# Kernel tuning notes

Hardware: AMD Instinct MI355X
Metric: run time of the kernel (lower is better)

The kernel has to match this reference:

```python
import jax, jax.numpy as jnp
import numpy as np

B, T, C, H = 4, 1024, 1024, 16
D = C // H  # head dim = 64


def setup_inputs() -> dict:
    key = jax.random.key(0)
    ks = jax.random.split(key, 12)
    s = 1.0 / np.sqrt(C)
    inp = {
        "x": jax.random.normal(ks[0], (B, T, C), jnp.float32),
        "Wq": jax.random.normal(ks[1], (C, C), jnp.float32) * s,
        "bq": jnp.zeros((C,), jnp.float32),
        "Wk": jax.random.normal(ks[2], (C, C), jnp.float32) * s,
        "bk": jnp.zeros((C,), jnp.float32),
        "Wv": jax.random.normal(ks[3], (C, C), jnp.float32) * s,
        "bv": jnp.zeros((C,), jnp.float32),
        "time_weighting": jnp.ones((H, T, T), jnp.float32),
        "head_mix_w": jax.random.normal(ks[4], (H, H), jnp.float32) * (1.0 / np.sqrt(H)),
        "Wp": jax.random.normal(ks[5], (C, C), jnp.float32) * s,
        "bp": jnp.zeros((C,), jnp.float32),
    }
    return inp


def reference(x, Wq, bq, Wk, bk, Wv, bv, time_weighting, head_mix_w, Wp, bp):
    Bx, Tx, Cx = x.shape
    half = Cx // 2
    # time_shift: first half of channels sees x shifted by one step (row 0 -> zeros)
    x_shift = jnp.pad(x, ((0, 0), (1, 0), (0, 0)))[:, :Tx, :half]
    xs = jnp.concatenate([x_shift, x[:, :, half:]], axis=-1)

    def heads(y):  # [B,T,C] -> [B,H,T,D]
        return y.reshape(Bx, Tx, H, D).transpose(0, 2, 1, 3)

    q = heads(xs @ Wq.T + bq)
    k = heads(xs @ Wk.T + bk)
    v = heads(xs @ Wv.T + bv)

    att = jnp.einsum("bhtd,bhsd->bhts", q, k) * (1.0 / np.sqrt(D))
    causal = jnp.tril(jnp.ones((Tx, Tx), bool))
    att = jnp.where(causal, att, -jnp.inf)
    att = jax.nn.softmax(att, axis=-1)
    att = att * time_weighting[:, :Tx, :Tx]
    # 1x1 conv across heads
    att = jnp.einsum("oh,bhts->bots", head_mix_w, att)

    y = jnp.einsum("bhts,bhsd->bhtd", att, v)
    y = y.transpose(0, 2, 1, 3).reshape(Bx, Tx, Cx)
    return y @ Wp.T + bp
```

## Files before the change

### kernel.cpp

```cpp
#include <hip/hip_runtime.h>
#include <hip/hip_bf16.h>

#define T_ 1024

typedef __attribute__((ext_vector_type(8))) short short8;
typedef __attribute__((ext_vector_type(4))) float f32x4;
typedef __bf16 bf16x8 __attribute__((ext_vector_type(8)));
typedef __attribute__((ext_vector_type(4))) unsigned short ushort4v;

__device__ __forceinline__ unsigned short f2bf(float f) {
    unsigned u = __float_as_uint(f);
    u += 0x7fffu + ((u >> 16) & 1u);
    return (unsigned short)(u >> 16);
}
__device__ __forceinline__ float bf2f(unsigned short s) {
    return __uint_as_float(((unsigned)s) << 16);
}
__device__ __forceinline__ unsigned short f2h(float f) {
    _Float16 h = (_Float16)f;
    return __builtin_bit_cast(unsigned short, h);
}
__device__ __forceinline__ float h2f(unsigned short u) {
    return (float)__builtin_bit_cast(_Float16, u);
}

__device__ __forceinline__ void gload16(const unsigned short* g, unsigned short* l) {
    __builtin_amdgcn_global_load_lds((const __attribute__((address_space(1))) unsigned int*)g,
                                     (__attribute__((address_space(3))) unsigned int*)l,
                                     16, 0, 0);
}

__global__ __launch_bounds__(256) void k_convert(
    const float* __restrict__ s0, const float* __restrict__ s1,
    const float* __restrict__ s2, const float* __restrict__ s3,
    unsigned short* __restrict__ d0, unsigned short* __restrict__ d1,
    unsigned short* __restrict__ d2, unsigned short* __restrict__ d3) {
    const float* src; unsigned short* dst;
    switch (blockIdx.y) {
        case 0:  src = s0; dst = d0; break;
        case 1:  src = s1; dst = d1; break;
        case 2:  src = s2; dst = d2; break;
        default: src = s3; dst = d3; break;
    }
    int i = (blockIdx.x * 256 + threadIdx.x) * 4;
    float4 v = *(const float4*)(src + i);
    ushort4v ov = { f2bf(v.x), f2bf(v.y), f2bf(v.z), f2bf(v.w) };
    *(ushort4v*)(dst + i) = ov;
}

__global__ __launch_bounds__(256) void k_xs(const float* __restrict__ x,
                                            unsigned short* __restrict__ xs) {
    int idx = (blockIdx.x * 256 + threadIdx.x) * 4;
    int c = idx & 1023;
    int m = idx >> 10;
    int t = m & 1023;
    float4 v;
    if (c < 512) {
        if (t == 0) { v.x = v.y = v.z = v.w = 0.f; }
        else        { v = *(const float4*)(x + (size_t)(m - 1) * 1024 + c); }
    } else {
        v = *(const float4*)(x + (size_t)m * 1024 + c);
    }
    ushort4v ov = { f2bf(v.x), f2bf(v.y), f2bf(v.z), f2bf(v.w) };
    *(ushort4v*)(xs + (size_t)m * 1024 + c) = ov;
}

__device__ __forceinline__ void gemm_body(const unsigned short* __restrict__ A,
                                          const unsigned short* __restrict__ Bt,
                                          int m0, int n0, int tid, f32x4 acc[4][4],
                                          unsigned short (*As)[32], unsigned short (*Bs)[32]) {
    const int lane = tid & 63, w = tid >> 6;
    const int wr = w >> 1, wc = w & 1;
    const int srow = lane >> 2;
    const int scp  = lane & 3;
#pragma unroll
    for (int i = 0; i < 4; i++)
#pragma unroll
        for (int j = 0; j < 4; j++) acc[i][j] = (f32x4){0.f, 0.f, 0.f, 0.f};

    for (int k0 = 0; k0 < 1024; k0 += 32) {
        __syncthreads();
#pragma unroll
        for (int it = 0; it < 2; it++) {
            int base = it * 64 + w * 16;
            int row = base + srow;
            int c2 = scp ^ ((row >> 1) & 3);
            gload16(A + (size_t)(m0 + row) * 1024 + k0 + c2 * 8, &As[base][0]);
            gload16(Bt + (size_t)(n0 + row) * 1024 + k0 + c2 * 8, &Bs[base][0]);
        }
        __syncthreads();
        bf16x8 af[4], bg[4];
        int c = lane >> 4;
#pragma unroll
        for (int i = 0; i < 4; i++) {
            int row = wr * 64 + i * 16 + (lane & 15);
            af[i] = *(const bf16x8*)&As[row][(c ^ ((row >> 1) & 3)) * 8];
        }
#pragma unroll
        for (int j = 0; j < 4; j++) {
            int row = wc * 64 + j * 16 + (lane & 15);
            bg[j] = *(const bf16x8*)&Bs[row][(c ^ ((row >> 1) & 3)) * 8];
        }
#pragma unroll
        for (int i = 0; i < 4; i++)
#pragma unroll
            for (int j = 0; j < 4; j++)
                acc[i][j] = __builtin_amdgcn_mfma_f32_16x16x32_bf16(af[i], bg[j], acc[i][j], 0, 0, 0);
    }
}

__global__ __launch_bounds__(256) void k_gemm_qkv(
    const unsigned short* __restrict__ A,
    const unsigned short* __restrict__ wq, const unsigned short* __restrict__ wk,
    const unsigned short* __restrict__ wv,
    const float* __restrict__ bq, const float* __restrict__ bk, const float* __restrict__ bv,
    unsigned short* __restrict__ qo, unsigned short* __restrict__ ko,
    unsigned short* __restrict__ vo) {
    __shared__ unsigned short As[128][32];
    __shared__ unsigned short Bs[128][32];
    const int mat = blockIdx.y >> 3;
    const unsigned short* Bt = mat == 0 ? wq : (mat == 1 ? wk : wv);
    const float* bias = mat == 0 ? bq : (mat == 1 ? bk : bv);
    unsigned short* out = mat == 0 ? qo : (mat == 1 ? ko : vo);
    const int m0 = blockIdx.x * 128, n0 = (blockIdx.y & 7) * 128;
    const int tid = threadIdx.x, lane = tid & 63, w = tid >> 6;
    const int wr = w >> 1, wc = w & 1;
    f32x4 acc[4][4];
    gemm_body(A, Bt, m0, n0, tid, acc, As, Bs);
#pragma unroll
    for (int i = 0; i < 4; i++) {
        int mbase = m0 + wr * 64 + i * 16 + ((lane >> 4) << 2);
#pragma unroll
        for (int j = 0; j < 4; j++) {
            int n = n0 + wc * 64 + j * 16 + (lane & 15);
            float bv_ = bias[n];
            int h = n >> 6, d = n & 63;
#pragma unroll
            for (int r = 0; r < 4; r++) {
                int mm = mbase + r;
                int b = mm >> 10, t = mm & 1023;
                out[(size_t)((b * 16 + h) * 1024 + t) * 64 + d] = f2bf(acc[i][j][r] + bv_);
            }
        }
    }
}

__global__ __launch_bounds__(256) void k_gemm_out(
    const unsigned short* __restrict__ A, const unsigned short* __restrict__ Bt,
    const float* __restrict__ bias, float* __restrict__ out) {
    __shared__ unsigned short As[128][32];
    __shared__ unsigned short Bs[128][32];
    const int m0 = blockIdx.x * 128, n0 = blockIdx.y * 128;
    const int tid = threadIdx.x, lane = tid & 63, w = tid >> 6;
    const int wr = w >> 1, wc = w & 1;
    f32x4 acc[4][4];
    gemm_body(A, Bt, m0, n0, tid, acc, As, Bs);
#pragma unroll
    for (int i = 0; i < 4; i++) {
        int mbase = m0 + wr * 64 + i * 16 + ((lane >> 4) << 2);
#pragma unroll
        for (int j = 0; j < 4; j++) {
            int n = n0 + wc * 64 + j * 16 + (lane & 15);
            float bv_ = bias[n];
#pragma unroll
            for (int r = 0; r < 4; r++)
                out[(size_t)(mbase + r) * 1024 + n] = acc[i][j][r] + bv_;
        }
    }
}

__global__ __launch_bounds__(256) void k_scores(const unsigned short* __restrict__ qb,
                                                const unsigned short* __restrict__ kb,
                                                unsigned short* __restrict__ Eb,
                                                float* __restrict__ invb) {
    __shared__ unsigned short qs[64][64];
    __shared__ unsigned short ks[64][64];
    const int tid = threadIdx.x, lane = tid & 63, w = tid >> 6;
    const int t0 = (15 - (int)blockIdx.x) * 64;
    const int bh = blockIdx.y;
    const unsigned short* qp = qb + (size_t)bh * 65536;
    const unsigned short* kp = kb + (size_t)bh * 65536;

#pragma unroll
    for (int it = 0; it < 2; it++) {
        int ch = it * 256 + tid; int row = ch >> 3, c = ch & 7;
        *(short8*)&qs[row][(c ^ (row & 7)) * 8] = *(const short8*)(qp + (size_t)(t0 + row) * 64 + c * 8);
    }
    __syncthreads();
    const int row_a = w * 16 + (lane & 15);
    bf16x8 a0 = *(const bf16x8*)&qs[row_a][(((lane >> 4)    ) ^ (row_a & 7)) * 8];
    bf16x8 a1 = *(const bf16x8*)&qs[row_a][(((lane >> 4) + 4) ^ (row_a & 7)) * 8];
    const int tr = t0 + w * 16 + ((lane >> 4) << 2);
    float l_[4] = {0.f, 0.f, 0.f, 0.f};
    unsigned short* ep = Eb + (size_t)bh * ((size_t)T_ * T_);

    for (int s0 = 0; s0 <= t0 + 63; s0 += 64) {
        __syncthreads();
#pragma unroll
        for (int it = 0; it < 2; it++) {
            int ch = it * 256 + tid; int row = ch >> 3, c = ch & 7;
            *(short8*)&ks[row][(c ^ (row & 7)) * 8] = *(const short8*)(kp + (size_t)(s0 + row) * 64 + c * 8);
        }
        __syncthreads();
        f32x4 S[4];
#pragma unroll
        for (int sf = 0; sf < 4; sf++) {
            int row = sf * 16 + (lane & 15);
            bf16x8 b0 = *(const bf16x8*)&ks[row][(((lane >> 4)    ) ^ (row & 7)) * 8];
            bf16x8 b1 = *(const bf16x8*)&ks[row][(((lane >> 4) + 4) ^ (row & 7)) * 8];
            f32x4 z = (f32x4){0.f, 0.f, 0.f, 0.f};
            z = __builtin_amdgcn_mfma_f32_16x16x32_bf16(a0, b0, z, 0, 0, 0);
            z = __builtin_amdgcn_mfma_f32_16x16x32_bf16(a1, b1, z, 0, 0, 0);
            S[sf] = z;
        }
#pragma unroll
        for (int sf = 0; sf < 4; sf++) {
            int s = s0 + sf * 16 + (lane & 15);
#pragma unroll
            for (int r = 0; r < 4; r++) {
                float es = (s <= tr + r) ? __expf(S[sf][r] * 0.125f) : 0.f;
                l_[r] += es;
                ep[(size_t)(tr + r) * T_ + s] = f2h(es);
            }
        }
    }
#pragma unroll
    for (int r = 0; r < 4; r++) {
        float ts = l_[r];
        ts += __shfl_xor(ts, 1);
        ts += __shfl_xor(ts, 2);
        ts += __shfl_xor(ts, 4);
        ts += __shfl_xor(ts, 8);
        l_[r] = ts;
    }
    if ((lane & 15) == 0) {
#pragma unroll
        for (int r = 0; r < 4; r++) invb[(size_t)bh * T_ + tr + r] = 1.f / l_[r];
    }
}

__global__ __launch_bounds__(256) void k_mix6(unsigned short* __restrict__ Sb,
                                              const float* __restrict__ invb,
                                              const float* __restrict__ tw,
                                              const float* __restrict__ mixw) {
    const int t = blockIdx.x, b = blockIdx.y;
    const int send = t | 63;
    const int tid = threadIdx.x;
    __shared__ float mw[256];
    __shared__ float inv_s[16];
    mw[tid] = mixw[tid];
    if (tid < 16) inv_s[tid] = invb[(size_t)(b * 16 + tid) * T_ + t];
    __syncthreads();

    const int s4 = tid * 4;
    if (s4 > send) return;
    unsigned short* plane0 = Sb + (size_t)b * 16 * 1048576;
    const unsigned rowb = (unsigned)t * 1024u + (unsigned)s4;

    ushort4v e[16];
    float4 tv[16];
#pragma unroll
    for (int h = 0; h < 16; h++)
        e[h] = *(const ushort4v*)(plane0 + (size_t)h * 1048576 + rowb);
#pragma unroll
    for (int h = 0; h < 16; h++)
        tv[h] = *(const float4*)(tw + (size_t)h * 1048576 + rowb);

    float p[16][4];
#pragma unroll
    for (int h = 0; h < 16; h++) {
        float iv = inv_s[h];
        p[h][0] = h2f(e[h].x) * iv * tv[h].x;
        p[h][1] = h2f(e[h].y) * iv * tv[h].y;
        p[h][2] = h2f(e[h].z) * iv * tv[h].z;
        p[h][3] = h2f(e[h].w) * iv * tv[h].w;
    }

#pragma unroll
    for (int o = 0; o < 16; o++) {
        float a0 = 0.f, a1 = 0.f, a2 = 0.f, a3 = 0.f;
#pragma unroll
        for (int h = 0; h < 16; h++) {
            float m = mw[o * 16 + h];
            a0 += m * p[h][0];
            a1 += m * p[h][1];
            a2 += m * p[h][2];
            a3 += m * p[h][3];
        }
        ushort4v pk = { f2bf(a0), f2bf(a1), f2bf(a2), f2bf(a3) };
        *(ushort4v*)(plane0 + (size_t)o * 1048576 + rowb) = pk;
    }
}

__global__ __launch_bounds__(256) void k_av(const unsigned short* __restrict__ att,
                                            const unsigned short* __restrict__ vb,
                                            unsigned short* __restrict__ y1) {
    __shared__ unsigned short as_[64][64];
    __shared__ unsigned short vs[64][72];
    const int tid = threadIdx.x, lane = tid & 63, w = tid >> 6;
    const int t0 = (15 - (int)blockIdx.x) * 64;
    const int bh = blockIdx.y;
    const int b = bh >> 4, h = bh & 15;
    const unsigned short* ap = att + (size_t)bh * 1048576;
    const unsigned short* vp = vb + (size_t)bh * 65536;
    f32x4 acc[4];
#pragma unroll
    for (int j = 0; j < 4; j++) acc[j] = (f32x4){0.f, 0.f, 0.f, 0.f};

    for (int s0 = 0; s0 <= t0 + 63; s0 += 64) {
        __syncthreads();
#pragma unroll
        for (int it = 0; it < 2; it++) {
            int ch = it * 256 + tid;
            int row = ch >> 3, c = ch & 7;
            *(short8*)&as_[row][(c ^ (row & 7)) * 8] =
                *(const short8*)(ap + (size_t)(t0 + row) * 1024 + s0 + c * 8);
            int sp = ch >> 3, dc = (ch & 7) * 8;
            short8 vv = *(const short8*)(vp + (size_t)(s0 + sp) * 64 + dc);
#pragma unroll
            for (int i = 0; i < 8; i++) vs[dc + i][sp] = ((unsigned short*)&vv)[i];
        }
        __syncthreads();
        const int row_a = w * 16 + (lane & 15);
#pragma unroll
        for (int ks = 0; ks < 2; ks++) {
            bf16x8 af = *(const bf16x8*)&as_[row_a][((((lane >> 4) + 4 * ks)) ^ (row_a & 7)) * 8];
#pragma unroll
            for (int j = 0; j < 4; j++) {
                bf16x8 bg = *(const bf16x8*)&vs[j * 16 + (lane & 15)][ks * 32 + (lane >> 4) * 8];
                acc[j] = __builtin_amdgcn_mfma_f32_16x16x32_bf16(af, bg, acc[j], 0, 0, 0);
            }
        }
    }

    int t = t0 + w * 16 + ((lane >> 4) << 2);
#pragma unroll
    for (int j = 0; j < 4; j++) {
        int d = j * 16 + (lane & 15);
#pragma unroll
        for (int r = 0; r < 4; r++)
            y1[(size_t)(b * 1024 + t + r) * 1024 + h * 64 + d] = f2bf(acc[j][r]);
    }
}

extern "C" void kernel_launch(void* const* d_in, const int* in_sizes, int n_in,
                              void* d_out, int out_size, void* d_ws, size_t ws_size,
                              hipStream_t stream) {
    (void)in_sizes; (void)n_in; (void)out_size; (void)ws_size;
    const float* x    = (const float*)d_in[0];
    const float* Wq   = (const float*)d_in[1];
    const float* bq   = (const float*)d_in[2];
    const float* Wk   = (const float*)d_in[3];
    const float* bk   = (const float*)d_in[4];
    const float* Wv   = (const float*)d_in[5];
    const float* bv   = (const float*)d_in[6];
    const float* tw   = (const float*)d_in[7];
    const float* mixw = (const float*)d_in[8];
    const float* Wp   = (const float*)d_in[9];
    const float* bp   = (const float*)d_in[10];

    char* ws = (char*)d_ws;
    size_t off = 0;
    auto alloc = [&](size_t bytes) -> char* {
        char* p = ws + off;
        off += (bytes + 255) & ~(size_t)255;
        return p;
    };
    unsigned short* xs  = (unsigned short*)alloc((size_t)4096 * 1024 * 2);
    unsigned short* wqb = (unsigned short*)alloc((size_t)1024 * 1024 * 2);
    unsigned short* wkb = (unsigned short*)alloc((size_t)1024 * 1024 * 2);
    unsigned short* wvb = (unsigned short*)alloc((size_t)1024 * 1024 * 2);
    unsigned short* wpb = (unsigned short*)alloc((size_t)1024 * 1024 * 2);
    unsigned short* qb  = (unsigned short*)alloc((size_t)64 * 1024 * 64 * 2);
    unsigned short* kb  = (unsigned short*)alloc((size_t)64 * 1024 * 64 * 2);
    unsigned short* vb_ = (unsigned short*)alloc((size_t)64 * 1024 * 64 * 2);
    unsigned short* Sb  = (unsigned short*)alloc((size_t)64 * 1024 * 1024 * 2);
    float*          invb = (float*)alloc((size_t)64 * 1024 * 4);
    unsigned short* y1  = (unsigned short*)alloc((size_t)4096 * 1024 * 2);

    k_convert<<<dim3(1024, 4), 256, 0, stream>>>(Wq, Wk, Wv, Wp, wqb, wkb, wvb, wpb);
    k_xs<<<4096, 256, 0, stream>>>(x, xs);
    k_gemm_qkv<<<dim3(32, 24), 256, 0, stream>>>(xs, wqb, wkb, wvb, bq, bk, bv, qb, kb, vb_);
    k_scores<<<dim3(16, 64), 256, 0, stream>>>(qb, kb, Sb, invb);
    k_mix6<<<dim3(1024, 4), 256, 0, stream>>>(Sb, invb, tw, mixw);
    k_av<<<dim3(16, 64), 256, 0, stream>>>(Sb, vb_, y1);
    k_gemm_out<<<dim3(32, 8), 256, 0, stream>>>(y1, wpb, bp, (float*)d_out);
}
```

Before: 322.4 us.

## Store V transposed from QKV GEMM and load V fragments directly in AV

The QKV projection now writes V in a [bh][d][t] transposed layout, so the attention-times-V kernel can read MFMA B fragments straight from global memory. This removes the shared-memory V tile and its scalar transposing stores. The cost is strided 2-byte global stores in the GEMM epilogue for V, plus uncoalesced global fragment loads in k_av. Separately, the head-mix kernel's grid is reordered so that consecutive blocks walk batch before time, which changes the order in which the large score planes are touched.

```diff
diff --git a/kernel.cpp b/kernel.cpp
--- a/kernel.cpp
+++ b/kernel.cpp
@@ -139,7 +139,10 @@
             for (int r = 0; r < 4; r++) {
                 int mm = mbase + r;
                 int b = mm >> 10, t = mm & 1023;
-                out[(size_t)((b * 16 + h) * 1024 + t) * 64 + d] = f2bf(acc[i][j][r] + bv_);
+                size_t idx = (mat == 2)
+                    ? (size_t)((b * 16 + h) * 64 + d) * 1024 + t
+                    : (size_t)((b * 16 + h) * 1024 + t) * 64 + d;
+                out[idx] = f2bf(acc[i][j][r] + bv_);
             }
         }
     }
@@ -243,7 +246,7 @@
                                               const float* __restrict__ invb,
                                               const float* __restrict__ tw,
                                               const float* __restrict__ mixw) {
-    const int t = blockIdx.x, b = blockIdx.y;
+    const int b = blockIdx.x, t = blockIdx.y;
     const int send = t | 63;
     const int tid = threadIdx.x;
     __shared__ float mw[256];
@@ -293,19 +296,21 @@
 }
 
 __global__ __launch_bounds__(256) void k_av(const unsigned short* __restrict__ att,
-                                            const unsigned short* __restrict__ vb,
+                                            const unsigned short* __restrict__ vt,
                                             unsigned short* __restrict__ y1) {
     __shared__ unsigned short as_[64][64];
-    __shared__ unsigned short vs[64][72];
     const int tid = threadIdx.x, lane = tid & 63, w = tid >> 6;
     const int t0 = (15 - (int)blockIdx.x) * 64;
     const int bh = blockIdx.y;
     const int b = bh >> 4, h = bh & 15;
     const unsigned short* ap = att + (size_t)bh * 1048576;
-    const unsigned short* vp = vb + (size_t)bh * 65536;
+    const unsigned short* vp = vt + (size_t)bh * 65536;
     f32x4 acc[4];
 #pragma unroll
     for (int j = 0; j < 4; j++) acc[j] = (f32x4){0.f, 0.f, 0.f, 0.f};
+    const int row_a = w * 16 + (lane & 15);
+    const int dofs = (lane & 15);
+    const int kofs = (lane >> 4) * 8;
 
     for (int s0 = 0; s0 <= t0 + 63; s0 += 64) {
         __syncthreads();
@@ -315,21 +320,21 @@
             int row = ch >> 3, c = ch & 7;
             *(short8*)&as_[row][(c ^ (row & 7)) * 8] =
                 *(const short8*)(ap + (size_t)(t0 + row) * 1024 + s0 + c * 8);
-            int sp = ch >> 3, dc = (ch & 7) * 8;
-            short8 vv = *(const short8*)(vp + (size_t)(s0 + sp) * 64 + dc);
-#pragma unroll
-            for (int i = 0; i < 8; i++) vs[dc + i][sp] = ((unsigned short*)&vv)[i];
-        }
-        __syncthreads();
-        const int row_a = w * 16 + (lane & 15);
+        }
+        bf16x8 bg[2][4];
+#pragma unroll
+        for (int ks = 0; ks < 2; ks++)
+#pragma unroll
+            for (int j = 0; j < 4; j++)
+                bg[ks][j] = *(const bf16x8*)(vp + (size_t)(j * 16 + dofs) * 1024
+                                             + s0 + ks * 32 + kofs);
+        __syncthreads();
 #pragma unroll
         for (int ks = 0; ks < 2; ks++) {
             bf16x8 af = *(const bf16x8*)&as_[row_a][((((lane >> 4) + 4 * ks)) ^ (row_a & 7)) * 8];
 #pragma unroll
-            for (int j = 0; j < 4; j++) {
-                bf16x8 bg = *(const bf16x8*)&vs[j * 16 + (lane & 15)][ks * 32 + (lane >> 4) * 8];
-                acc[j] = __builtin_amdgcn_mfma_f32_16x16x32_bf16(af, bg, acc[j], 0, 0, 0);
-            }
+            for (int j = 0; j < 4; j++)
+                acc[j] = __builtin_amdgcn_mfma_f32_16x16x32_bf16(af, bg[ks][j], acc[j], 0, 0, 0);
         }
     }
 
@@ -373,16 +378,16 @@
     unsigned short* wpb = (unsigned short*)alloc((size_t)1024 * 1024 * 2);
     unsigned short* qb  = (unsigned short*)alloc((size_t)64 * 1024 * 64 * 2);
     unsigned short* kb  = (unsigned short*)alloc((size_t)64 * 1024 * 64 * 2);
-    unsigned short* vb_ = (unsigned short*)alloc((size_t)64 * 1024 * 64 * 2);
+    unsigned short* vtb = (unsigned short*)alloc((size_t)64 * 1024 * 64 * 2);
     unsigned short* Sb  = (unsigned short*)alloc((size_t)64 * 1024 * 1024 * 2);
     float*          invb = (float*)alloc((size_t)64 * 1024 * 4);
     unsigned short* y1  = (unsigned short*)alloc((size_t)4096 * 1024 * 2);
 
     k_convert<<<dim3(1024, 4), 256, 0, stream>>>(Wq, Wk, Wv, Wp, wqb, wkb, wvb, wpb);
     k_xs<<<4096, 256, 0, stream>>>(x, xs);
-    k_gemm_qkv<<<dim3(32, 24), 256, 0, stream>>>(xs, wqb, wkb, wvb, bq, bk, bv, qb, kb, vb_);
+    k_gemm_qkv<<<dim3(32, 24), 256, 0, stream>>>(xs, wqb, wkb, wvb, bq, bk, bv, qb, kb, vtb);
     k_scores<<<dim3(16, 64), 256, 0, stream>>>(qb, kb, Sb, invb);
-    k_mix6<<<dim3(1024, 4), 256, 0, stream>>>(Sb, invb, tw, mixw);
-    k_av<<<dim3(16, 64), 256, 0, stream>>>(Sb, vb_, y1);
+    k_mix6<<<dim3(4, 1024), 256, 0, stream>>>(Sb, invb, tw, mixw);
+    k_av<<<dim3(16, 64), 256, 0, stream>>>(Sb, vtb, y1);
     k_gemm_out<<<dim3(32, 8), 256, 0, stream>>>(y1, wpb, bp, (float*)d_out);
 }
```

Measured after the change: 340.5 us. +5.6%, slower.
